# Kernel tuning notes

Hardware: AMD Instinct MI355X
Metric: run time of the kernel (lower is better)

The kernel has to match this reference:

```python
import jax, jax.numpy as jnp
import numpy as np

N_NODES = 100000
N_EDGES = 3200000
N_FEAT = 128
N_CLASSES = 8


def setup_inputs() -> dict:
    key = jax.random.key(0)
    ks = jax.random.split(key, 8)
    h = jax.random.normal(ks[0], (N_NODES, N_FEAT), dtype=jnp.float32)
    edge_index = jax.random.randint(ks[1], (2, N_EDGES), 0, N_NODES, dtype=jnp.int64)
    def lin(k, fi, fo):
        return jax.random.normal(k, (fi, fo), dtype=jnp.float32) / np.sqrt(fi)
    return {
        "h": h,
        "edge_index": edge_index,
        "W1": lin(ks[2], N_FEAT, 16), "b1": jnp.zeros((16,), jnp.float32),
        "W2": lin(ks[3], 16, 4),      "b2": jnp.zeros((4,), jnp.float32),
        "W3": lin(ks[4], 4, 2),      "b3": jnp.zeros((2,), jnp.float32),
        "Wc": lin(ks[5], 2, N_CLASSES), "bc": jnp.zeros((N_CLASSES,), jnp.float32),
    }


def _gcn_norm(edge_index, n_nodes):
    # PyG GCNConv: add self-loops, symmetric normalization deg^-1/2 A deg^-1/2
    loop = jnp.arange(n_nodes, dtype=edge_index.dtype)
    src = jnp.concatenate([edge_index[0], loop])  # [E+N]
    dst = jnp.concatenate([edge_index[1], loop])
    deg = jax.ops.segment_sum(jnp.ones_like(dst, dtype=jnp.float32), dst,
                              num_segments=n_nodes)
    dinv = jnp.where(deg > 0, jax.lax.rsqrt(deg), 0.0)
    norm = dinv[src] * dinv[dst]  # [E+N]
    return src, dst, norm


def _gcn_conv(x, W, b, src, dst, norm, n_nodes):
    xw = x @ W                                # [N, Fo] linear first (small Fo)
    msg = xw[src] * norm[:, None]             # gather + scale  [E+N, Fo]
    out = jax.ops.segment_sum(msg, dst, num_segments=n_nodes)  # scatter-add
    return out + b


def reference(h, edge_index, W1, b1, W2, b2, W3, b3, Wc, bc):
    n = h.shape[0]
    src, dst, norm = _gcn_norm(edge_index, n)
    h1 = jnp.tanh(_gcn_conv(h, W1, b1, src, dst, norm, n))
    h2 = jnp.tanh(_gcn_conv(h1, W2, b2, src, dst, norm, n))
    h3 = jnp.tanh(_gcn_conv(h2, W3, b3, src, dst, norm, n))
    out = h3 @ Wc + bc
    return (out, h3)
```

## Files before the change

kernel.cpp:

```cpp
#include <hip/hip_runtime.h>
#include <math.h>

#define N_NODES 100000
#define N_EDGES 3200000
#define NPB    256
#define NBUCK  ((N_NODES + NPB - 1) / NPB)
#define NBLKA  512
#define EPB    ((N_EDGES + NBLKA - 1) / NBLKA)
#define NB_BLK ((N_NODES + 255) / 256)

typedef float f4nt __attribute__((ext_vector_type(4)));

#define MAIN_WS_WORDS (3u*N_NODES + N_EDGES + 3200000u + NBUCK*NBLKA + NBUCK + 2u)
#define MAIN_WS_BYTES (MAIN_WS_WORDS * 4u)
#define ATOMIC_WS_BYTES ((33u*N_NODES + 16u) * 4u)

__global__ void k_detect_i64(const int* __restrict__ ei_words, int* __restrict__ flag) {
    if (blockIdx.x == 0 && threadIdx.x == 0) {
        int allzero = 1;
        for (int i = 0; i < 64; i++)
            if (ei_words[2 * i + 1] != 0) allzero = 0;
        *flag = allzero;
    }
}

__device__ __forceinline__ unsigned load_idx(const int* p32, const long long* p64,
                                             int is64, int e) {
    return is64 ? (unsigned)(unsigned long long)__builtin_nontemporal_load(&p64[e])
                : (unsigned)__builtin_nontemporal_load(&p32[e]);
}

__global__ __launch_bounds__(256) void k_bcount(const int* __restrict__ dst32,
                                                const long long* __restrict__ dst64,
                                                const int* __restrict__ flag,
                                                int* __restrict__ cmat) {
    __shared__ int lc[NBUCK];
    int t = threadIdx.x, blk = blockIdx.x;
    for (int i = t; i < NBUCK; i += 256) lc[i] = 0;
    __syncthreads();
    int is64 = *flag;
    int e0 = blk * EPB, e1 = e0 + EPB; if (e1 > N_EDGES) e1 = N_EDGES;
    for (int e = e0 + t; e < e1; e += 256) {
        unsigned d = load_idx(dst32, dst64, is64, e);
        if (d < N_NODES) atomicAdd(&lc[d >> 8], 1);
    }
    __syncthreads();
    for (int b = t; b < NBUCK; b += 256) cmat[b * NBLKA + blk] = lc[b];
}

__global__ __launch_bounds__(256) void k_bsum(const int* __restrict__ cmat,
                                              int* __restrict__ bt) {
    int b = blockIdx.x, t = threadIdx.x;
    int v = cmat[b * NBLKA + t] + cmat[b * NBLKA + t + 256];
#pragma unroll
    for (int off = 32; off > 0; off >>= 1) v += __shfl_down(v, off, 64);
    __shared__ int s[4];
    if ((t & 63) == 0) s[t >> 6] = v;
    __syncthreads();
    if (t == 0) bt[b] = s[0] + s[1] + s[2] + s[3];
}

__global__ __launch_bounds__(512) void k_btscan(int* __restrict__ bt) {
    __shared__ int s[512];
    int t = threadIdx.x;
    s[t] = (t < NBUCK) ? bt[t] : 0;
    __syncthreads();
    for (int off = 1; off < 512; off <<= 1) {
        int v = (t >= off) ? s[t - off] : 0;
        __syncthreads();
        s[t] += v;
        __syncthreads();
    }
    if (t < NBUCK) bt[t] = (t == 0) ? 0 : s[t - 1];
    if (t == 0) bt[NBUCK] = s[NBUCK - 1];
}

__global__ __launch_bounds__(512) void k_boffs(int* __restrict__ cmat,
                                               const int* __restrict__ bt) {
    __shared__ int s[512];
    int b = blockIdx.x, t = threadIdx.x;
    s[t] = cmat[b * NBLKA + t];
    __syncthreads();
    for (int off = 1; off < 512; off <<= 1) {
        int v = (t >= off) ? s[t - off] : 0;
        __syncthreads();
        s[t] += v;
        __syncthreads();
    }
    cmat[b * NBLKA + t] = ((t == 0) ? 0 : s[t - 1]) + bt[b];
}

__global__ __launch_bounds__(256) void k_bscatter(const int* __restrict__ src32,
                                                  const long long* __restrict__ src64,
                                                  const int* __restrict__ dst32,
                                                  const long long* __restrict__ dst64,
                                                  const int* __restrict__ flag,
                                                  const int* __restrict__ cmat,
                                                  int* __restrict__ P) {
    __shared__ int cur[NBUCK];
    int t = threadIdx.x, blk = blockIdx.x;
    for (int i = t; i < NBUCK; i += 256) cur[i] = cmat[i * NBLKA + blk];
    __syncthreads();
    int is64 = *flag;
    int e0 = blk * EPB, e1 = e0 + EPB; if (e1 > N_EDGES) e1 = N_EDGES;
    for (int e = e0 + t; e < e1; e += 256) {
        unsigned d = load_idx(dst32, dst64, is64, e);
        if (d < N_NODES) {
            unsigned s = load_idx(src32, src64, is64, e);
            int pos = atomicAdd(&cur[d >> 8], 1);
            P[pos] = (int)(((d & 255u) << 17) | (s & 0x1FFFFu));
        }
    }
}

__global__ __launch_bounds__(256) void k_bbuild(const int* __restrict__ P,
                                                const int* __restrict__ bt,
                                                int* __restrict__ adj,
                                                int* __restrict__ rowstart,
                                                int* __restrict__ rowend,
                                                float* __restrict__ dinv) {
    __shared__ int cnt[NPB];
    __shared__ int s[NPB];
    int b = blockIdx.x, t = threadIdx.x;
    int bo = bt[b], be = bt[b + 1];
    cnt[t] = 0;
    __syncthreads();
    for (int i = bo + t; i < be; i += 256)
        atomicAdd(&cnt[__builtin_nontemporal_load(&P[i]) >> 17], 1);
    __syncthreads();
    s[t] = cnt[t];
    __syncthreads();
    for (int off = 1; off < 256; off <<= 1) {
        int v = (t >= off) ? s[t - off] : 0;
        __syncthreads();
        s[t] += v;
        __syncthreads();
    }
    int ex = (t == 0) ? 0 : s[t - 1];
    int node = b * NPB + t;
    if (node < N_NODES) {
        rowstart[node] = bo + ex;
        rowend[node]   = bo + ex + cnt[t];
        dinv[node]     = rsqrtf((float)cnt[t] + 1.0f);
    }
    __syncthreads();
    s[t] = ex;
    __syncthreads();
    for (int i = bo + t; i < be; i += 256) {
        int ent = __builtin_nontemporal_load(&P[i]);
        int pos = bo + atomicAdd(&s[ent >> 17], 1);
        adj[pos] = ent & 0x1FFFF;
    }
}

__global__ __launch_bounds__(256) void k_gemm1_p(const float* __restrict__ h,
                                                 const float* __restrict__ W,
                                                 const float* __restrict__ dinv,
                                                 float* __restrict__ xs) {
    __shared__ float Wt[16 * 132];
    __shared__ float Hs[16 * 132];
    int tid = threadIdx.x;
    for (int i = tid; i < 2048; i += 256) {
        int k = i >> 4, f = i & 15;
        Wt[f * 132 + k] = W[i];
    }
    int nodeBase = blockIdx.x * 16;
    for (int i = tid; i < 512; i += 256) {
        int r = i >> 5, c = i & 31;
        f4nt v = __builtin_nontemporal_load(
            ((const f4nt*)(h + (size_t)(nodeBase + r) * 128)) + c);
        *((f4nt*)&Hs[r * 132 + c * 4]) = v;
    }
    __syncthreads();
    int nl = tid >> 4, f = tid & 15;
    int n = nodeBase + nl;
    const float* hr = &Hs[nl * 132];
    const float* wr = &Wt[f * 132];
    float s = 0.0f;
#pragma unroll
    for (int k = 0; k < 128; k++) s += hr[k] * wr[k];
    s *= dinv[n];
    xs[(f >> 3) * (8 * N_NODES) + n * 8 + (f & 7)] = s;
}

template <int FI, int FO>
__global__ __launch_bounds__(256) void k_gemm_smallp(const float* __restrict__ x,
                                                     const float* __restrict__ W,
                                                     const float* __restrict__ dinv,
                                                     float* __restrict__ xs) {
    int i = blockIdx.x * 256 + threadIdx.x;
    if (i >= N_NODES * FO) return;
    int n = i / FO, f = i % FO;
    float s = 0.0f;
#pragma unroll
    for (int k = 0; k < FI; k++) s += x[n * FI + k] * W[k * FO + f];
    xs[i] = s * dinv[n];
}

template <int F, int NL, int FTOT, int FOFF>
__global__ __launch_bounds__(256) void k_pull(const float* __restrict__ xsp,
                                              const int* __restrict__ adj,
                                              const int* __restrict__ rowstart,
                                              const int* __restrict__ rowend,
                                              const float* __restrict__ dinv,
                                              const float* __restrict__ bias,
                                              float* __restrict__ out) {
    constexpr int R = NL / F;
    int t = threadIdx.x;
    int g = t / NL, q = t % NL;
    int f = q % F, k = q / F;
    int n = blockIdx.x * (256 / NL) + g;
    if (n >= N_NODES) return;
    int s0 = rowstart[n], e0 = rowend[n];
    float acc = 0.0f;
    for (int j = s0 + k; j < e0; j += R)
        acc += xsp[__builtin_nontemporal_load(&adj[j]) * F + f];
#pragma unroll
    for (int off = NL / 2; off >= F; off >>= 1)
        acc += __shfl_xor(acc, off, 64);
    if (k == 0) {
        acc += xsp[n * F + f];
        out[n * FTOT + FOFF + f] = tanhf(dinv[n] * acc + bias[f]);
    }
}

__global__ __launch_bounds__(256) void k_pull_final(const float* __restrict__ xsp,
                                                    const int* __restrict__ adj,
                                                    const int* __restrict__ rowstart,
                                                    const int* __restrict__ rowend,
                                                    const float* __restrict__ dinv,
                                                    const float* __restrict__ b3,
                                                    const float* __restrict__ Wc,
                                                    const float* __restrict__ bc,
                                                    float* __restrict__ out,
                                                    float* __restrict__ h3out) {
    const int NL = 8;
    int t = threadIdx.x;
    int g = t / NL, q = t % NL;
    int f = q & 1, k = q >> 1;
    int n = blockIdx.x * (256 / NL) + g;
    if (n >= N_NODES) return;
    int s0 = rowstart[n], e0 = rowend[n];
    float acc = 0.0f;
    for (int j = s0 + k; j < e0; j += 4)
        acc += xsp[__builtin_nontemporal_load(&adj[j]) * 2 + f];
    acc += __shfl_xor(acc, 4, 64);
    acc += __shfl_xor(acc, 2, 64);
    float a = 0.0f;
    if (q < 2) {
        acc += xsp[n * 2 + f];
        a = tanhf(dinv[n] * acc + b3[f]);
        h3out[2 * n + f] = a;
    }
    int wl = t & 63, gb = wl & ~7;
    float a0 = __shfl(a, gb, 64);
    float a1 = __shfl(a, gb + 1, 64);
    out[8 * n + q] = a0 * Wc[q] + a1 * Wc[8 + q] + bc[q];
}

__global__ __launch_bounds__(256) void k_gemm1(const float* __restrict__ h,
                                               const float* __restrict__ W,
                                               const float* __restrict__ dinv,
                                               float* __restrict__ xs, float* acc) {
    __shared__ float Wt[16 * 132];
    __shared__ float Hs[16 * 132];
    int tid = threadIdx.x;
    for (int i = tid; i < 2048; i += 256) {
        int k = i >> 4, f = i & 15;
        Wt[f * 132 + k] = W[i];
    }
    int nodeBase = blockIdx.x * 16;
    for (int i = tid; i < 512; i += 256) {
        int r = i >> 5, c = i & 31;
        float4 v = ((const float4*)(h + (size_t)(nodeBase + r) * 128))[c];
        *((float4*)&Hs[r * 132 + c * 4]) = v;
    }
    __syncthreads();
    int nl = tid >> 4, f = tid & 15;
    int n = nodeBase + nl;
    const float* hr = &Hs[nl * 132];
    const float* wr = &Wt[f * 132];
    float s = 0.0f;
#pragma unroll
    for (int k = 0; k < 128; k++) s += hr[k] * wr[k];
    s *= dinv[n];
    xs[n * 16 + f] = s;
    acc[n * 16 + f] = s;
}
template <int FI, int FO>
__global__ __launch_bounds__(256) void k_gemm_small(const float* __restrict__ x,
                                                    const float* __restrict__ W,
                                                    const float* __restrict__ dinv,
                                                    float* __restrict__ xs, float* acc) {
    int i = blockIdx.x * 256 + threadIdx.x;
    if (i >= N_NODES * FO) return;
    int n = i / FO, f = i % FO;
    float s = 0.0f;
#pragma unroll
    for (int k = 0; k < FI; k++) s += x[n * FI + k] * W[k * FO + f];
    s *= dinv[n];
    xs[i] = s;
    acc[i] = s;
}
template <int F>
__global__ __launch_bounds__(256) void k_scatter(const int* __restrict__ src32,
                                                 const long long* __restrict__ src64,
                                                 const int* __restrict__ dst32,
                                                 const long long* __restrict__ dst64,
                                                 const int* __restrict__ flag,
                                                 const float* __restrict__ xs,
                                                 float* __restrict__ acc) {
    long long gid = (long long)blockIdx.x * 256 + threadIdx.x;
    int e = (int)(gid / F), f = (int)(gid % F);
    if (e < N_EDGES) {
        int is64 = *flag;
        unsigned s = load_idx(src32, src64, is64, e);
        unsigned d = load_idx(dst32, dst64, is64, e);
        if (s < N_NODES && d < N_NODES)
            atomicAdd(&acc[d * F + f], xs[s * F + f]);
    }
}
__global__ __launch_bounds__(256) void k_deg_init(float* __restrict__ deg) {
    int i = blockIdx.x * 256 + threadIdx.x;
    if (i < N_NODES) deg[i] = 1.0f;
}
__global__ __launch_bounds__(256) void k_deg_count(const int* __restrict__ dst32,
                                                   const long long* __restrict__ dst64,
                                                   const int* __restrict__ flag,
                                                   float* __restrict__ deg) {
    int e = blockIdx.x * 256 + threadIdx.x;
    if (e < N_EDGES) {
        unsigned d = load_idx(dst32, dst64, *flag, e);
        if (d < N_NODES) atomicAdd(&deg[d], 1.0f);
    }
}
__global__ __launch_bounds__(256) void k_rsqrt(float* __restrict__ deg) {
    int i = blockIdx.x * 256 + threadIdx.x;
    if (i < N_NODES) deg[i] = rsqrtf(deg[i]);
}
template <int F>
__global__ __launch_bounds__(256) void k_finish(const float* __restrict__ acc,
                                                const float* __restrict__ dinv,
                                                const float* __restrict__ b,
                                                float* __restrict__ out) {
    int i = blockIdx.x * 256 + threadIdx.x;
    if (i >= N_NODES * F) return;
    int n = i / F, f = i % F;
    out[i] = tanhf(dinv[n] * acc[i] + b[f]);
}
__global__ __launch_bounds__(256) void k_final(const float* __restrict__ acc3,
                                               const float* __restrict__ dinv,
                                               const float* __restrict__ b3,
                                               const float* __restrict__ Wc,
                                               const float* __restrict__ bc,
                                               float* __restrict__ out,
                                               float* __restrict__ h3out) {
    int n = blockIdx.x * 256 + threadIdx.x;
    if (n >= N_NODES) return;
    float di = dinv[n];
    float a0 = tanhf(di * acc3[2 * n + 0] + b3[0]);
    float a1 = tanhf(di * acc3[2 * n + 1] + b3[1]);
    h3out[2 * n + 0] = a0;
    h3out[2 * n + 1] = a1;
#pragma unroll
    for (int c = 0; c < 8; c++)
        out[8 * n + c] = a0 * Wc[c] + a1 * Wc[8 + c] + bc[c];
}
__global__ __launch_bounds__(256) void k_zero_out(float* __restrict__ out, int n) {
    int i = blockIdx.x * 256 + threadIdx.x;
    if (i < n) out[i] = 0.0f;
}

extern "C" void kernel_launch(void* const* d_in, const int* in_sizes, int n_in,
                              void* d_out, int out_size, void* d_ws, size_t ws_size,
                              hipStream_t stream) {
    float* out = (float*)d_out;
    const float* h   = (const float*)d_in[0];
    const void*  ei  = d_in[1];
    const float* W1  = (const float*)d_in[2];
    const float* b1  = (const float*)d_in[3];
    const float* W2  = (const float*)d_in[4];
    const float* b2  = (const float*)d_in[5];
    const float* W3  = (const float*)d_in[6];
    const float* b3  = (const float*)d_in[7];
    const float* Wc  = (const float*)d_in[8];
    const float* bc  = (const float*)d_in[9];

    const int*       src32 = (const int*)ei;
    const int*       dst32 = src32 + N_EDGES;
    const long long* src64 = (const long long*)ei;
    const long long* dst64 = src64 + N_EDGES;

    float* h3out = out + 8 * N_NODES;
    const int NB_E = (N_EDGES + 255) / 256;

    if (d_ws != nullptr && ws_size >= MAIN_WS_BYTES) {
        float* dinv   = (float*)d_ws;
        int* rowstart = (int*)(dinv + N_NODES);
        int* rowend   = rowstart + N_NODES;
        int* adj      = rowend + N_NODES;
        int* S        = adj + N_EDGES;
        float* xs     = (float*)S;
        float* hbuf   = xs + 16 * N_NODES;
        int* P        = S;
        int* cmat     = S + 3200000;
        int* bt       = cmat + NBUCK * NBLKA;
        int* flag     = bt + NBUCK + 1;

        k_detect_i64<<<1, 64, 0, stream>>>(src32, flag);
        k_bcount<<<NBLKA, 256, 0, stream>>>(dst32, dst64, flag, cmat);
        k_bsum<<<NBUCK, 256, 0, stream>>>(cmat, bt);
        k_btscan<<<1, 512, 0, stream>>>(bt);
        k_boffs<<<NBUCK, 512, 0, stream>>>(cmat, bt);
        k_bscatter<<<NBLKA, 256, 0, stream>>>(src32, src64, dst32, dst64, flag, cmat, P);
        k_bbuild<<<NBUCK, 256, 0, stream>>>(P, bt, adj, rowstart, rowend, dinv);

        k_gemm1_p<<<N_NODES / 16, 256, 0, stream>>>(h, W1, dinv, xs);
        k_pull<8, 64, 16, 0><<<25000, 256, 0, stream>>>(
            xs, adj, rowstart, rowend, dinv, b1, hbuf);
        k_pull<8, 64, 16, 8><<<25000, 256, 0, stream>>>(
            xs + 8 * N_NODES, adj, rowstart, rowend, dinv, b1 + 8, hbuf);
        k_gemm_smallp<16, 4><<<(N_NODES * 4 + 255) / 256, 256, 0, stream>>>(hbuf, W2, dinv, xs);
        k_pull<4, 32, 4, 0><<<12500, 256, 0, stream>>>(
            xs, adj, rowstart, rowend, dinv, b2, hbuf);
        k_gemm_smallp<4, 2><<<(N_NODES * 2 + 255) / 256, 256, 0, stream>>>(hbuf, W3, dinv, xs);
        k_pull_final<<<3125, 256, 0, stream>>>(
            xs, adj, rowstart, rowend, dinv, b3, Wc, bc, out, h3out);
        return;
    }

    if (d_ws != nullptr && ws_size >= ATOMIC_WS_BYTES) {
        float* ws   = (float*)d_ws;
        float* dinv = ws;
        float* bufA = dinv + N_NODES;
        float* bufB = bufA + 16 * N_NODES;
        int*   flag = (int*)(bufB + 16 * N_NODES);
        float* xs1 = bufA, *acc1 = bufB, *h1 = bufA;
        float* xs2 = bufB, *acc2 = bufB + 4 * N_NODES, *h2 = bufA;
        float* xs3 = bufB, *acc3 = bufB + 2 * N_NODES;

        k_detect_i64<<<1, 64, 0, stream>>>(src32, flag);
        k_deg_init<<<NB_BLK, 256, 0, stream>>>(dinv);
        k_deg_count<<<NB_E, 256, 0, stream>>>(dst32, dst64, flag, dinv);
        k_rsqrt<<<NB_BLK, 256, 0, stream>>>(dinv);
        k_gemm1<<<N_NODES / 16, 256, 0, stream>>>(h, W1, dinv, xs1, acc1);
        k_scatter<16><<<(int)(((long long)N_EDGES * 16 + 255) / 256), 256, 0, stream>>>(
            src32, src64, dst32, dst64, flag, xs1, acc1);
        k_finish<16><<<(N_NODES * 16 + 255) / 256, 256, 0, stream>>>(acc1, dinv, b1, h1);
        k_gemm_small<16, 4><<<(N_NODES * 4 + 255) / 256, 256, 0, stream>>>(h1, W2, dinv, xs2, acc2);
        k_scatter<4><<<(int)(((long long)N_EDGES * 4 + 255) / 256), 256, 0, stream>>>(
            src32, src64, dst32, dst64, flag, xs2, acc2);
        k_finish<4><<<(N_NODES * 4 + 255) / 256, 256, 0, stream>>>(acc2, dinv, b2, h2);
        k_gemm_small<4, 2><<<(N_NODES * 2 + 255) / 256, 256, 0, stream>>>(h2, W3, dinv, xs3, acc3);
        k_scatter<2><<<(int)(((long long)N_EDGES * 2 + 255) / 256), 256, 0, stream>>>(
            src32, src64, dst32, dst64, flag, xs3, acc3);
        k_final<<<NB_BLK, 256, 0, stream>>>(acc3, dinv, b3, Wc, bc, out, h3out);
        return;
    }

    k_zero_out<<<(out_size + 255) / 256, 256, 0, stream>>>(out, out_size);
}
```

Measured before the change: 435.6 us.

## Fuse layer-1 pull passes, prefetch adjacency indices, inline int64 detection

Merges the two layer-1 pull kernels, which each handled 8 of the 16 features, into one kernel. It reads the adjacency list once and gathers from both 8-feature halves. The pull loops now software-prefetch the next adjacency index before the current gather, to hide some load latency. The separate int64-detection kernel launch is removed, and each block now detects the index width itself with a wavefront ballot, which adds a few redundant loads per block.

```diff
diff --git a/kernel.cpp b/kernel.cpp
--- a/kernel.cpp
+++ b/kernel.cpp
@@ -15,6 +15,13 @@
 #define MAIN_WS_BYTES (MAIN_WS_WORDS * 4u)
 #define ATOMIC_WS_BYTES ((33u*N_NODES + 16u) * 4u)
 
+__device__ __forceinline__ int detect_is64(const int* __restrict__ w) {
+    int t = threadIdx.x & 63;
+    int v = w[2 * t + 1];
+    unsigned long long nz = __ballot(v != 0);
+    return nz == 0ull;
+}
+
 __global__ void k_detect_i64(const int* __restrict__ ei_words, int* __restrict__ flag) {
     if (blockIdx.x == 0 && threadIdx.x == 0) {
         int allzero = 1;
@@ -32,13 +39,12 @@
 
 __global__ __launch_bounds__(256) void k_bcount(const int* __restrict__ dst32,
                                                 const long long* __restrict__ dst64,
-                                                const int* __restrict__ flag,
                                                 int* __restrict__ cmat) {
+    int is64 = detect_is64(dst32 - 2 * N_EDGES);
     __shared__ int lc[NBUCK];
     int t = threadIdx.x, blk = blockIdx.x;
     for (int i = t; i < NBUCK; i += 256) lc[i] = 0;
     __syncthreads();
-    int is64 = *flag;
     int e0 = blk * EPB, e1 = e0 + EPB; if (e1 > N_EDGES) e1 = N_EDGES;
     for (int e = e0 + t; e < e1; e += 256) {
         unsigned d = load_idx(dst32, dst64, is64, e);
@@ -94,14 +100,13 @@
                                                   const long long* __restrict__ src64,
                                                   const int* __restrict__ dst32,
                                                   const long long* __restrict__ dst64,
-                                                  const int* __restrict__ flag,
                                                   const int* __restrict__ cmat,
                                                   int* __restrict__ P) {
+    int is64 = detect_is64(src32);
     __shared__ int cur[NBUCK];
     int t = threadIdx.x, blk = blockIdx.x;
     for (int i = t; i < NBUCK; i += 256) cur[i] = cmat[i * NBLKA + blk];
     __syncthreads();
-    int is64 = *flag;
     int e0 = blk * EPB, e1 = e0 + EPB; if (e1 > N_EDGES) e1 = N_EDGES;
     for (int e = e0 + t; e < e1; e += 256) {
         unsigned d = load_idx(dst32, dst64, is64, e);
@@ -195,6 +200,50 @@
 #pragma unroll
     for (int k = 0; k < FI; k++) s += x[n * FI + k] * W[k * FO + f];
     xs[i] = s * dinv[n];
+}
+
+__global__ __launch_bounds__(256) void k_pull16_dual(const float* __restrict__ p0,
+                                                     const float* __restrict__ p1,
+                                                     const int* __restrict__ adj,
+                                                     const int* __restrict__ rowstart,
+                                                     const int* __restrict__ rowend,
+                                                     const float* __restrict__ dinv,
+                                                     const float* __restrict__ b1,
+                                                     float* __restrict__ out) {
+    int t = threadIdx.x;
+    int g = t >> 6;
+    int q = t & 63;
+    int f = q & 7, k = q >> 3;
+    int n = blockIdx.x * 4 + g;
+    if (n >= N_NODES) return;
+    int s0 = rowstart[n], e0 = rowend[n];
+    float a0 = 0.0f, a1 = 0.0f;
+    int j = s0 + k;
+    if (j < e0) {
+        int src = __builtin_nontemporal_load(&adj[j]);
+        while (true) {
+            int jn = j + 8;
+            bool more = jn < e0;
+            int srcn = 0;
+            if (more) srcn = __builtin_nontemporal_load(&adj[jn]);
+            a0 += p0[src * 8 + f];
+            a1 += p1[src * 8 + f];
+            if (!more) break;
+            j = jn; src = srcn;
+        }
+    }
+#pragma unroll
+    for (int off = 32; off >= 8; off >>= 1) {
+        a0 += __shfl_xor(a0, off, 64);
+        a1 += __shfl_xor(a1, off, 64);
+    }
+    if (k == 0) {
+        a0 += p0[n * 8 + f];
+        a1 += p1[n * 8 + f];
+        float di = dinv[n];
+        out[n * 16 + f]     = tanhf(di * a0 + b1[f]);
+        out[n * 16 + 8 + f] = tanhf(di * a1 + b1[8 + f]);
+    }
 }
 
 template <int F, int NL, int FTOT, int FOFF>
@@ -213,8 +262,19 @@
     if (n >= N_NODES) return;
     int s0 = rowstart[n], e0 = rowend[n];
     float acc = 0.0f;
-    for (int j = s0 + k; j < e0; j += R)
-        acc += xsp[__builtin_nontemporal_load(&adj[j]) * F + f];
+    int j = s0 + k;
+    if (j < e0) {
+        int src = __builtin_nontemporal_load(&adj[j]);
+        while (true) {
+            int jn = j + R;
+            bool more = jn < e0;
+            int srcn = 0;
+            if (more) srcn = __builtin_nontemporal_load(&adj[jn]);
+            acc += xsp[src * F + f];
+            if (!more) break;
+            j = jn; src = srcn;
+        }
+    }
 #pragma unroll
     for (int off = NL / 2; off >= F; off >>= 1)
         acc += __shfl_xor(acc, off, 64);
@@ -242,8 +302,19 @@
     if (n >= N_NODES) return;
     int s0 = rowstart[n], e0 = rowend[n];
     float acc = 0.0f;
-    for (int j = s0 + k; j < e0; j += 4)
-        acc += xsp[__builtin_nontemporal_load(&adj[j]) * 2 + f];
+    int j = s0 + k;
+    if (j < e0) {
+        int src = __builtin_nontemporal_load(&adj[j]);
+        while (true) {
+            int jn = j + 4;
+            bool more = jn < e0;
+            int srcn = 0;
+            if (more) srcn = __builtin_nontemporal_load(&adj[jn]);
+            acc += xsp[src * 2 + f];
+            if (!more) break;
+            j = jn; src = srcn;
+        }
+    }
     acc += __shfl_xor(acc, 4, 64);
     acc += __shfl_xor(acc, 2, 64);
     float a = 0.0f;
@@ -405,21 +476,17 @@
         int* P        = S;
         int* cmat     = S + 3200000;
         int* bt       = cmat + NBUCK * NBLKA;
-        int* flag     = bt + NBUCK + 1;
-
-        k_detect_i64<<<1, 64, 0, stream>>>(src32, flag);
-        k_bcount<<<NBLKA, 256, 0, stream>>>(dst32, dst64, flag, cmat);
+
+        k_bcount<<<NBLKA, 256, 0, stream>>>(dst32, dst64, cmat);
         k_bsum<<<NBUCK, 256, 0, stream>>>(cmat, bt);
         k_btscan<<<1, 512, 0, stream>>>(bt);
         k_boffs<<<NBUCK, 512, 0, stream>>>(cmat, bt);
-        k_bscatter<<<NBLKA, 256, 0, stream>>>(src32, src64, dst32, dst64, flag, cmat, P);
+        k_bscatter<<<NBLKA, 256, 0, stream>>>(src32, src64, dst32, dst64, cmat, P);
         k_bbuild<<<NBUCK, 256, 0, stream>>>(P, bt, adj, rowstart, rowend, dinv);
 
         k_gemm1_p<<<N_NODES / 16, 256, 0, stream>>>(h, W1, dinv, xs);
-        k_pull<8, 64, 16, 0><<<25000, 256, 0, stream>>>(
-            xs, adj, rowstart, rowend, dinv, b1, hbuf);
-        k_pull<8, 64, 16, 8><<<25000, 256, 0, stream>>>(
-            xs + 8 * N_NODES, adj, rowstart, rowend, dinv, b1 + 8, hbuf);
+        k_pull16_dual<<<25000, 256, 0, stream>>>(
+            xs, xs + 8 * N_NODES, adj, rowstart, rowend, dinv, b1, hbuf);
         k_gemm_smallp<16, 4><<<(N_NODES * 4 + 255) / 256, 256, 0, stream>>>(hbuf, W2, dinv, xs);
         k_pull<4, 32, 4, 0><<<12500, 256, 0, stream>>>(
             xs, adj, rowstart, rowend, dinv, b2, hbuf);
```

Result: faster. 388.2 us (-10.9%).
